# Performance work log

Measured on AMD Instinct MI355X. Metric: run time of the kernel, lower is better.

Reference implementation:

```python
import jax, jax.numpy as jnp
import numpy as np

EMBED_DIM = 2048
HEAD_DIM = 128
B, T = 4, 2048


def setup_inputs() -> dict:
    key = jax.random.key(0)
    k1, k2, k3, k4 = jax.random.split(key, 4)
    x_in = jax.random.normal(k1, (B, T, EMBED_DIM), dtype=jnp.float32)
    scale = 1.0 / np.sqrt(EMBED_DIM)
    Wq = jax.random.normal(k2, (EMBED_DIM, HEAD_DIM), dtype=jnp.float32) * scale
    Wk = jax.random.normal(k3, (EMBED_DIM, HEAD_DIM), dtype=jnp.float32) * scale
    Wv = jax.random.normal(k4, (EMBED_DIM, HEAD_DIM), dtype=jnp.float32) * scale
    return {"x_in": x_in, "Wq": Wq, "Wk": Wk, "Wv": Wv}


def reference(x_in, Wq, Wk, Wv):
    # x_in: [B, T, E]; projections (Linear, no bias)
    q = jnp.einsum('bte,ed->btd', x_in, Wq)  # [B,T,D]
    k = jnp.einsum('bte,ed->btd', x_in, Wk)
    v = jnp.einsum('bte,ed->btd', x_in, Wv)
    t = x_in.shape[1]
    d = Wq.shape[1]
    s = jnp.einsum('btd,bsd->bts', q, k) / jnp.sqrt(jnp.asarray(d, q.dtype))  # [B,Tq,Tk]
    # causal mask: positions with tril==0 (k index > q index) -> -inf
    causal = jnp.tril(jnp.ones((t, t), dtype=bool))
    s = jnp.where(causal, s, -jnp.inf)
    # NOTE: original module applies softmax over dim=1 (query axis), faithfully reproduced
    a = jax.nn.softmax(s, axis=1)
    z = jnp.einsum('bts,bsd->btd', a, v)  # [B,T,D]
    return z
```

## Files before the change

kernel.cpp:

```cpp
#include <hip/hip_runtime.h>

typedef _Float16 f16x8 __attribute__((ext_vector_type(8)));
typedef _Float16 f16x4 __attribute__((ext_vector_type(4)));
typedef float f32x4 __attribute__((ext_vector_type(4)));

#define T_DIM 2048
#define E_DIM 2048
#define D_DIM 128
#define NB 4
#define KSP_P 4
#define KCH_P 512
#define KSP_A 8
#define KCH_A 256
#define NCH2 32

__device__ __forceinline__ void gll16(const void* g, void* l) {
  __builtin_amdgcn_global_load_lds(
      (const __attribute__((address_space(1))) unsigned int*)g,
      (__attribute__((address_space(3))) unsigned int*)l, 16, 0, 0);
}

__device__ __forceinline__ void merge_stat(float& m, float& l, float pm, float pl) {
  if (pm != -__builtin_inff()) {
    float nm = fmaxf(m, pm);
    l = l * __expf(m - nm) + pl * __expf(pm - nm);
    m = nm;
  }
}


__global__ void cvt_w(const float* __restrict__ Wq, const float* __restrict__ Wk,
                      const float* __restrict__ Wv, _Float16* __restrict__ WhT) {
  int idx = blockIdx.x * 256 + threadIdx.x;
  int w = blockIdx.y;
  const float* W = (w == 0) ? Wq : ((w == 1) ? Wk : Wv);
  int e = idx & (E_DIM - 1), d = idx >> 11;
  WhT[(size_t)w * (D_DIM * E_DIM) + idx] = (_Float16)W[e * D_DIM + d];
}


__global__ __launch_bounds__(256) void proj_gemm(
    const float* __restrict__ x, const _Float16* __restrict__ WhT,
    _Float16* __restrict__ Ph) {
  __shared__ float Asw[128 * 32];
  __shared__ _Float16 Bsw[128 * 32];
  const int tid = threadIdx.x, w = tid >> 6, lane = tid & 63;
  const int wr = w >> 1, wc = w & 1, quad = lane >> 4, l16 = lane & 15;
  const int t0 = blockIdx.x * 128;
  const int wsel = blockIdx.y, ks = blockIdx.z;
  const _Float16* B = WhT + (size_t)wsel * (D_DIM * E_DIM);
  const int arow = tid >> 3, aseg = tid & 7;
  const int brow = tid >> 2, bseg = tid & 3;
  f32x4 acc[4][4] = {};
  for (int k0 = ks * KCH_P; k0 < ks * KCH_P + KCH_P; k0 += 32) {
    __syncthreads();
#pragma unroll
    for (int p = 0; p < 4; ++p) {
      int row = p * 32 + arow;
      int gseg = aseg ^ (row & 7);
      gll16(x + (size_t)(t0 + row) * E_DIM + k0 + gseg * 4,
            Asw + row * 32 + aseg * 4);
    }
#pragma unroll
    for (int p = 0; p < 2; ++p) {
      int row = p * 64 + brow;
      int gseg = bseg ^ ((row >> 1) & 3);
      gll16(B + (size_t)row * E_DIM + k0 + gseg * 8,
            Bsw + row * 32 + bseg * 8);
    }
    __syncthreads();
    f16x8 af[4], bf[4];
#pragma unroll
    for (int i = 0; i < 4; ++i) {
      int row = wr * 64 + i * 16 + l16;
      int s0 = (2 * quad) ^ (row & 7);
      int s1 = (2 * quad + 1) ^ (row & 7);
      f32x4 a0 = *(const f32x4*)(Asw + row * 32 + s0 * 4);
      f32x4 a1 = *(const f32x4*)(Asw + row * 32 + s1 * 4);
#pragma unroll
      for (int e = 0; e < 4; ++e) {
        af[i][e] = (_Float16)a0[e];
        af[i][e + 4] = (_Float16)a1[e];
      }
    }
#pragma unroll
    for (int j = 0; j < 4; ++j) {
      int row = wc * 64 + j * 16 + l16;
      int sg = quad ^ ((row >> 1) & 3);
      bf[j] = *(const f16x8*)(Bsw + row * 32 + sg * 8);
    }
#pragma unroll
    for (int i = 0; i < 4; ++i)
#pragma unroll
      for (int j = 0; j < 4; ++j)
        acc[i][j] = __builtin_amdgcn_mfma_f32_16x16x32_f16(af[i], bf[j], acc[i][j], 0, 0, 0);
  }
  _Float16* P = Ph + ((size_t)(ks * 3 + wsel) << 20);
  if (wsel < 2) {
#pragma unroll
    for (int i = 0; i < 4; ++i)
#pragma unroll
      for (int j = 0; j < 4; ++j) {
        int n = wc * 64 + j * 16 + l16;
#pragma unroll
        for (int r = 0; r < 4; ++r) {
          int t = t0 + wr * 64 + i * 16 + quad * 4 + r;
          P[(size_t)t * D_DIM + n] = (_Float16)acc[i][j][r];
        }
      }
  } else {
#pragma unroll
    for (int i = 0; i < 4; ++i)
#pragma unroll
      for (int j = 0; j < 4; ++j) {
        int n = wc * 64 + j * 16 + l16;
        int t = t0 + wr * 64 + i * 16 + quad * 4;
        f16x4 o;
#pragma unroll
        for (int r = 0; r < 4; ++r) o[r] = (_Float16)acc[i][j][r];
        *(f16x4*)(P + ((size_t)(t >> 11) * D_DIM + n) * T_DIM + (t & (T_DIM - 1))) = o;
      }
  }
}


__global__ void proj_reduce(const _Float16* __restrict__ Ph, _Float16* __restrict__ Qh,
                            _Float16* __restrict__ Kh, _Float16* __restrict__ VT) {
  size_t u = ((size_t)blockIdx.x * 256 + threadIdx.x) * 8;
  int mat = (int)(u >> 20);
  size_t rem = u & ((1u << 20) - 1);
  float s[8] = {};
#pragma unroll
  for (int ks = 0; ks < KSP_P; ++ks) {
    f16x8 p = *(const f16x8*)(Ph + ((size_t)(ks * 3 + mat) << 20) + rem);
#pragma unroll
    for (int e = 0; e < 8; ++e) s[e] += (float)p[e];
  }
  f16x8 o;
#pragma unroll
  for (int e = 0; e < 8; ++e) o[e] = (_Float16)s[e];
  _Float16* dst = (mat == 0) ? Qh : ((mat == 1) ? Kh : VT);
  *(f16x8*)(dst + rem) = o;
}


__global__ __launch_bounds__(256) void s_gemm(const _Float16* __restrict__ Qh,
                                              const _Float16* __restrict__ Kh,
                                              _Float16* __restrict__ S,
                                              float* __restrict__ Pm,
                                              float* __restrict__ Pl) {
  int idx = blockIdx.x;
  int xt = (int)((sqrtf(8.f * idx + 1.f) - 1.f) * 0.5f);
  while ((xt + 1) * (xt + 2) / 2 <= idx) ++xt;
  while (xt * (xt + 1) / 2 > idx) --xt;
  int yt = idx - xt * (xt + 1) / 2;
  __shared__ _Float16 Bs[4][128 * 32];
  const int tid = threadIdx.x, w = tid >> 6, lane = tid & 63;
  const int wr = w >> 1, wc = w & 1, quad = lane >> 4, l16 = lane & 15;
  const int t0 = xt * 128, s0 = yt * 128, b = blockIdx.y;
  const _Float16* A = Qh + (size_t)b * T_DIM * D_DIM;
  const _Float16* B = Kh + (size_t)b * T_DIM * D_DIM;
  const int srow = lane >> 2;
  const int swz = ((lane & 3) ^ ((srow >> 1) & 3)) * 8;
#pragma unroll
  for (int kq = 0; kq < 4; ++kq)
#pragma unroll
    for (int q = 0; q < 2; ++q) {
      int rbase = w * 32 + q * 16;
      gll16(B + (size_t)(s0 + rbase + srow) * D_DIM + kq * 32 + swz,
            Bs[kq] + rbase * 32);
    }
  __syncthreads();
  f32x4 acc[4][4] = {};
  const int bsg = (quad ^ ((l16 >> 1) & 3)) * 8;
#pragma unroll
  for (int kq = 0; kq < 4; ++kq) {
    f16x8 af[4], bf[4];
#pragma unroll
    for (int i = 0; i < 4; ++i)
      af[i] = *(const f16x8*)(A + (size_t)(t0 + wr * 64 + i * 16 + l16) * D_DIM +
                              kq * 32 + quad * 8);
#pragma unroll
    for (int j = 0; j < 4; ++j)
      bf[j] = *(const f16x8*)(Bs[kq] + (wc * 64 + j * 16 + l16) * 32 + bsg);
#pragma unroll
    for (int i = 0; i < 4; ++i)
#pragma unroll
      for (int j = 0; j < 4; ++j)
        acc[i][j] = __builtin_amdgcn_mfma_f32_16x16x32_f16(af[i], bf[j], acc[i][j], 0, 0, 0);
  }
  _Float16* Sb = S + (size_t)b * T_DIM * T_DIM;
  const float scale = 0.08838834764831845f;
  const float NEG = -__builtin_inff();
#pragma unroll
  for (int j = 0; j < 4; ++j) {
    const int s = s0 + wc * 64 + j * 16 + l16;
    float m = NEG;
#pragma unroll
    for (int i = 0; i < 4; ++i)
#pragma unroll
      for (int r = 0; r < 4; ++r) {
        int t = t0 + wr * 64 + i * 16 + quad * 4 + r;
        float v = (s > t) ? NEG : acc[i][j][r] * scale;
        Sb[(size_t)t * T_DIM + s] = (_Float16)v;
        m = fmaxf(m, v);
      }
    float l = 0.f;
    if (m != NEG) {
#pragma unroll
      for (int i = 0; i < 4; ++i)
#pragma unroll
        for (int r = 0; r < 4; ++r) {
          int t = t0 + wr * 64 + i * 16 + quad * 4 + r;
          float v = (s > t) ? NEG : acc[i][j][r] * scale;
          l += __expf(v - m);
        }
    }
#pragma unroll
    for (int d = 16; d <= 32; d <<= 1) {
      float pm = __shfl_xor(m, d, 64);
      float pl = __shfl_xor(l, d, 64);
      merge_stat(m, l, pm, pl);
    }
    if (quad == 0) {
      int c = 2 * xt + wr;
      Pm[((size_t)c * NB + b) * T_DIM + s] = m;
      Pl[((size_t)c * NB + b) * T_DIM + s] = l;
    }
  }
}


__global__ __launch_bounds__(256) void comb_stats(const float* __restrict__ Pm,
                                                  const float* __restrict__ Pl,
                                                  float* __restrict__ M,
                                                  float* __restrict__ L) {
  __shared__ float sM[8][32];
  __shared__ float sL[8][32];
  const int g = threadIdx.x >> 5, sl = threadIdx.x & 31;
  const int c = blockIdx.x * 32 + sl;
  const int b = c >> 11, s = c & (T_DIM - 1);
  float m = -__builtin_inff(), l = 0.f;
#pragma unroll
  for (int k = 0; k < NCH2 / 8; ++k) {
    int ch = g * (NCH2 / 8) + k;
    if (ch >= (s >> 6)) {
      size_t idx = ((size_t)ch * NB + b) * T_DIM + s;
      merge_stat(m, l, Pm[idx], Pl[idx]);
    }
  }
  sM[g][sl] = m;
  sL[g][sl] = l;
  __syncthreads();
  if (threadIdx.x < 32) {
    const int c2 = blockIdx.x * 32 + threadIdx.x;
    float fm = -__builtin_inff(), fl = 0.f;
#pragma unroll
    for (int gg = 0; gg < 8; ++gg) merge_stat(fm, fl, sM[gg][threadIdx.x], sL[gg][threadIdx.x]);
    M[c2] = fm;
    L[c2] = 1.f / fl;
  }
}


__global__ __launch_bounds__(256) void av_gemm(const _Float16* __restrict__ S,
                                               const _Float16* __restrict__ VT,
                                               const float* __restrict__ M,
                                               const float* __restrict__ L,
                                               float* __restrict__ Zp) {
  const int t0 = blockIdx.x * 128, b = blockIdx.y, ks = blockIdx.z;
  const int Kmax = t0 + 128;
  const int Kstart = ks * KCH_A;
  if (Kstart >= Kmax) return;
  const int Kend = (Kstart + KCH_A < Kmax) ? (Kstart + KCH_A) : Kmax;
  __shared__ _Float16 As[128 * 32];
  __shared__ _Float16 Bs[128 * 32];
  __shared__ float Ms[KCH_A];
  __shared__ float Ls[KCH_A];
  const int tid = threadIdx.x, w = tid >> 6, lane = tid & 63;
  const int wr = w >> 1, wc = w & 1, quad = lane >> 4, l16 = lane & 15;
  const _Float16* Sb = S + (size_t)b * T_DIM * T_DIM;
  const _Float16* Vb = VT + (size_t)b * D_DIM * T_DIM;
  for (int i = tid; i < Kend - Kstart; i += 256) {
    Ms[i] = M[b * T_DIM + Kstart + i];
    Ls[i] = L[b * T_DIM + Kstart + i];
  }
  const int srow = lane >> 2, scol = (lane & 3) * 8;
  f32x4 acc[4][4] = {};
  for (int k0 = Kstart; k0 < Kend; k0 += 32) {
    __syncthreads();
#pragma unroll
    for (int q = 0; q < 2; ++q) {
      int u = q * 256 + tid;
      int row = u >> 2, c8 = (u & 3) * 8;
      int sc = k0 + c8;
      f16x8 v = *(const f16x8*)(Sb + (size_t)(t0 + row) * T_DIM + sc);
      f16x8 o;
#pragma unroll
      for (int e = 0; e < 8; ++e) {
        int li = sc + e - Kstart;
        float a = __expf((float)v[e] - Ms[li]) * Ls[li];
        o[e] = (_Float16)a;
      }
      *(f16x8*)(As + row * 32 + c8) = o;
      int rbase = w * 32 + q * 16;
      gll16(Vb + (size_t)(rbase + srow) * T_DIM + k0 + scol, Bs + rbase * 32);
    }
    __syncthreads();
    f16x8 af[4], bf[4];
#pragma unroll
    for (int i = 0; i < 4; ++i)
      af[i] = *(const f16x8*)(As + (wr * 64 + i * 16 + l16) * 32 + quad * 8);
#pragma unroll
    for (int j = 0; j < 4; ++j)
      bf[j] = *(const f16x8*)(Bs + (wc * 64 + j * 16 + l16) * 32 + quad * 8);
#pragma unroll
    for (int i = 0; i < 4; ++i)
#pragma unroll
      for (int j = 0; j < 4; ++j)
        acc[i][j] = __builtin_amdgcn_mfma_f32_16x16x32_f16(af[i], bf[j], acc[i][j], 0, 0, 0);
  }
  float* Zb = Zp + ((size_t)ks * NB + b) * T_DIM * D_DIM;
#pragma unroll
  for (int i = 0; i < 4; ++i)
#pragma unroll
    for (int j = 0; j < 4; ++j) {
      int n = wc * 64 + j * 16 + l16;
#pragma unroll
      for (int r = 0; r < 4; ++r) {
        int t = t0 + wr * 64 + i * 16 + quad * 4 + r;
        Zb[(size_t)t * D_DIM + n] = acc[i][j][r];
      }
    }
}


__global__ void z_reduce(const float* __restrict__ Zp, float* __restrict__ Z) {
  size_t flat = ((size_t)blockIdx.x * 256 + threadIdx.x) * 4;
  int t = (int)((flat >> 7) & (T_DIM - 1));
  int ns = ((t >> 7) + 2) >> 1;
  f32x4 s = {};
  for (int ks = 0; ks < ns; ++ks) {
    f32x4 p = *(const f32x4*)(Zp + ((size_t)ks * NB * T_DIM * D_DIM) + flat);
    s += p;
  }
  *(f32x4*)(Z + flat) = s;
}


extern "C" void kernel_launch(void* const* d_in, const int* in_sizes, int n_in,
                              void* d_out, int out_size, void* d_ws, size_t ws_size,
                              hipStream_t stream) {
  const float* x = (const float*)d_in[0];
  const float* Wq = (const float*)d_in[1];
  const float* Wk = (const float*)d_in[2];
  const float* Wv = (const float*)d_in[3];
  char* ws = (char*)d_ws;
  float* Zp = (float*)(ws);
  _Float16* WhT = (_Float16*)(ws + 33554432);
  _Float16* Qh = (_Float16*)(ws + 35127296);
  _Float16* Kh = (_Float16*)(ws + 37224448);
  _Float16* VT = (_Float16*)(ws + 39321600);
  _Float16* S = (_Float16*)(ws + 41418752);
  _Float16* Ph = (_Float16*)(ws + 41418752);
  float* M = (float*)(ws + 74973184);
  float* L = (float*)(ws + 75005952);
  float* Pm = (float*)(ws + 75038720);
  float* Pl = (float*)(ws + 76087296);
  float* Z = (float*)d_out;

  cvt_w<<<dim3(1024, 3), 256, 0, stream>>>(Wq, Wk, Wv, WhT);
  proj_gemm<<<dim3(64, 3, KSP_P), 256, 0, stream>>>(x, WhT, Ph);
  proj_reduce<<<1536, 256, 0, stream>>>(Ph, Qh, Kh, VT);
  s_gemm<<<dim3(136, 4), 256, 0, stream>>>(Qh, Kh, S, Pm, Pl);
  comb_stats<<<256, 256, 0, stream>>>(Pm, Pl, M, L);
  av_gemm<<<dim3(16, 4, KSP_A), 256, 0, stream>>>(S, VT, M, L, Zp);
  z_reduce<<<1024, 256, 0, stream>>>(Zp, Z);
}
```

Baseline: 176.4 us.

## Double-buffer projection GEMM loads and stage S tile through LDS for coalesced stores

The projection GEMM now uses two LDS buffers, so the next K-slice's global-to-LDS load is issued before the current slice is computed, removing one barrier per iteration. The S GEMM writes its scaled, masked scores into a padded LDS tile (reusing the K buffer) and then writes each row to global memory as 16-byte vector stores, instead of scattered 2-byte stores. The cost is double the LDS in the projection kernel plus extra barriers and an LDS round trip in the S kernel. One thing to check: the double-buffered loop no longer waits for the prefetched async loads to finish before the barrier and reads, so correctness depends on the compiler inserting that wait.

```diff
diff --git a/kernel.cpp b/kernel.cpp
--- a/kernel.cpp
+++ b/kernel.cpp
@@ -13,6 +13,7 @@
 #define KSP_A 8
 #define KCH_A 256
 #define NCH2 32
+#define ST_LD 136
 
 __device__ __forceinline__ void gll16(const void* g, void* l) {
   __builtin_amdgcn_global_load_lds(
@@ -42,8 +43,8 @@
 __global__ __launch_bounds__(256) void proj_gemm(
     const float* __restrict__ x, const _Float16* __restrict__ WhT,
     _Float16* __restrict__ Ph) {
-  __shared__ float Asw[128 * 32];
-  __shared__ _Float16 Bsw[128 * 32];
+  __shared__ float Asw[2][128 * 32];
+  __shared__ _Float16 Bsw[2][128 * 32];
   const int tid = threadIdx.x, w = tid >> 6, lane = tid & 63;
   const int wr = w >> 1, wc = w & 1, quad = lane >> 4, l16 = lane & 15;
   const int t0 = blockIdx.x * 128;
@@ -51,32 +52,38 @@
   const _Float16* B = WhT + (size_t)wsel * (D_DIM * E_DIM);
   const int arow = tid >> 3, aseg = tid & 7;
   const int brow = tid >> 2, bseg = tid & 3;
+  const int kstart = ks * KCH_P, kend = kstart + KCH_P;
+
+#define STAGE(bufi, kk)                                                   \
+  do {                                                                    \
+    _Pragma("unroll") for (int p = 0; p < 4; ++p) {                       \
+      int row = p * 32 + arow;                                            \
+      int gseg = aseg ^ (row & 7);                                        \
+      gll16(x + (size_t)(t0 + row) * E_DIM + (kk) + gseg * 4,             \
+            Asw[bufi] + row * 32 + aseg * 4);                             \
+    }                                                                     \
+    _Pragma("unroll") for (int p = 0; p < 2; ++p) {                       \
+      int row = p * 64 + brow;                                            \
+      int gseg = bseg ^ ((row >> 1) & 3);                                 \
+      gll16(B + (size_t)row * E_DIM + (kk) + gseg * 8,                    \
+            Bsw[bufi] + row * 32 + bseg * 8);                             \
+    }                                                                     \
+  } while (0)
+
+  STAGE(0, kstart);
   f32x4 acc[4][4] = {};
-  for (int k0 = ks * KCH_P; k0 < ks * KCH_P + KCH_P; k0 += 32) {
+  int buf = 0;
+  for (int k0 = kstart; k0 < kend; k0 += 32) {
     __syncthreads();
-#pragma unroll
-    for (int p = 0; p < 4; ++p) {
-      int row = p * 32 + arow;
-      int gseg = aseg ^ (row & 7);
-      gll16(x + (size_t)(t0 + row) * E_DIM + k0 + gseg * 4,
-            Asw + row * 32 + aseg * 4);
-    }
-#pragma unroll
-    for (int p = 0; p < 2; ++p) {
-      int row = p * 64 + brow;
-      int gseg = bseg ^ ((row >> 1) & 3);
-      gll16(B + (size_t)row * E_DIM + k0 + gseg * 8,
-            Bsw + row * 32 + bseg * 8);
-    }
-    __syncthreads();
+    if (k0 + 32 < kend) STAGE(buf ^ 1, k0 + 32);
     f16x8 af[4], bf[4];
 #pragma unroll
     for (int i = 0; i < 4; ++i) {
       int row = wr * 64 + i * 16 + l16;
       int s0 = (2 * quad) ^ (row & 7);
       int s1 = (2 * quad + 1) ^ (row & 7);
-      f32x4 a0 = *(const f32x4*)(Asw + row * 32 + s0 * 4);
-      f32x4 a1 = *(const f32x4*)(Asw + row * 32 + s1 * 4);
+      f32x4 a0 = *(const f32x4*)(Asw[buf] + row * 32 + s0 * 4);
+      f32x4 a1 = *(const f32x4*)(Asw[buf] + row * 32 + s1 * 4);
 #pragma unroll
       for (int e = 0; e < 4; ++e) {
         af[i][e] = (_Float16)a0[e];
@@ -87,14 +94,16 @@
     for (int j = 0; j < 4; ++j) {
       int row = wc * 64 + j * 16 + l16;
       int sg = quad ^ ((row >> 1) & 3);
-      bf[j] = *(const f16x8*)(Bsw + row * 32 + sg * 8);
+      bf[j] = *(const f16x8*)(Bsw[buf] + row * 32 + sg * 8);
     }
 #pragma unroll
     for (int i = 0; i < 4; ++i)
 #pragma unroll
       for (int j = 0; j < 4; ++j)
         acc[i][j] = __builtin_amdgcn_mfma_f32_16x16x32_f16(af[i], bf[j], acc[i][j], 0, 0, 0);
-  }
+    buf ^= 1;
+  }
+#undef STAGE
   _Float16* P = Ph + ((size_t)(ks * 3 + wsel) << 20);
   if (wsel < 2) {
 #pragma unroll
@@ -154,7 +163,9 @@
   while ((xt + 1) * (xt + 2) / 2 <= idx) ++xt;
   while (xt * (xt + 1) / 2 > idx) --xt;
   int yt = idx - xt * (xt + 1) / 2;
-  __shared__ _Float16 Bs[4][128 * 32];
+  __shared__ __align__(16) char smem[128 * ST_LD * 2];
+  _Float16* Bs = (_Float16*)smem;
+  _Float16* St = (_Float16*)smem;
   const int tid = threadIdx.x, w = tid >> 6, lane = tid & 63;
   const int wr = w >> 1, wc = w & 1, quad = lane >> 4, l16 = lane & 15;
   const int t0 = xt * 128, s0 = yt * 128, b = blockIdx.y;
@@ -168,7 +179,7 @@
     for (int q = 0; q < 2; ++q) {
       int rbase = w * 32 + q * 16;
       gll16(B + (size_t)(s0 + rbase + srow) * D_DIM + kq * 32 + swz,
-            Bs[kq] + rbase * 32);
+            Bs + kq * 4096 + rbase * 32);
     }
   __syncthreads();
   f32x4 acc[4][4] = {};
@@ -182,27 +193,28 @@
                               kq * 32 + quad * 8);
 #pragma unroll
     for (int j = 0; j < 4; ++j)
-      bf[j] = *(const f16x8*)(Bs[kq] + (wc * 64 + j * 16 + l16) * 32 + bsg);
+      bf[j] = *(const f16x8*)(Bs + kq * 4096 + (wc * 64 + j * 16 + l16) * 32 + bsg);
 #pragma unroll
     for (int i = 0; i < 4; ++i)
 #pragma unroll
       for (int j = 0; j < 4; ++j)
         acc[i][j] = __builtin_amdgcn_mfma_f32_16x16x32_f16(af[i], bf[j], acc[i][j], 0, 0, 0);
   }
-  _Float16* Sb = S + (size_t)b * T_DIM * T_DIM;
   const float scale = 0.08838834764831845f;
   const float NEG = -__builtin_inff();
+  __syncthreads();
 #pragma unroll
   for (int j = 0; j < 4; ++j) {
     const int s = s0 + wc * 64 + j * 16 + l16;
+    const int sloc = wc * 64 + j * 16 + l16;
     float m = NEG;
 #pragma unroll
     for (int i = 0; i < 4; ++i)
 #pragma unroll
       for (int r = 0; r < 4; ++r) {
-        int t = t0 + wr * 64 + i * 16 + quad * 4 + r;
-        float v = (s > t) ? NEG : acc[i][j][r] * scale;
-        Sb[(size_t)t * T_DIM + s] = (_Float16)v;
+        int tloc = wr * 64 + i * 16 + quad * 4 + r;
+        float v = (s > t0 + tloc) ? NEG : acc[i][j][r] * scale;
+        St[tloc * ST_LD + sloc] = (_Float16)v;
         m = fmaxf(m, v);
       }
     float l = 0.f;
@@ -211,8 +223,8 @@
       for (int i = 0; i < 4; ++i)
 #pragma unroll
         for (int r = 0; r < 4; ++r) {
-          int t = t0 + wr * 64 + i * 16 + quad * 4 + r;
-          float v = (s > t) ? NEG : acc[i][j][r] * scale;
+          int tloc = wr * 64 + i * 16 + quad * 4 + r;
+          float v = (s > t0 + tloc) ? NEG : acc[i][j][r] * scale;
           l += __expf(v - m);
         }
     }
@@ -227,6 +239,14 @@
       Pm[((size_t)c * NB + b) * T_DIM + s] = m;
       Pl[((size_t)c * NB + b) * T_DIM + s] = l;
     }
+  }
+  __syncthreads();
+  _Float16* Sb = S + (size_t)b * T_DIM * T_DIM;
+  const int rr = tid >> 1, hh = tid & 1;
+#pragma unroll
+  for (int e = 0; e < 8; ++e) {
+    f16x8 v = *(const f16x8*)(St + rr * ST_LD + hh * 64 + e * 8);
+    *(f16x8*)(Sb + (size_t)(t0 + rr) * T_DIM + s0 + hh * 64 + e * 8) = v;
   }
 }
 
```

Measured after the change: 177.9 us. About the same (+0.9%).
